# Optimization experiments

Measured on AMD Instinct MI355X. Metric: run time of the kernel, lower is better.

Reference implementation:

```python
import jax, jax.numpy as jnp
import numpy as np
import jax.scipy.linalg as jsl

EPS = 1e-3
GROUP_SIZE = 16

def setup_inputs() -> dict:
    key = jax.random.key(0)
    x = jax.random.normal(key, (32, 512, 56, 56), dtype=jnp.float32)
    return {"x": x}

def reference(x):
    B, C, H, W = x.shape
    gs = GROUP_SIZE
    G = C // gs
    # batch mean per channel: mean over (B, H, W)
    m = jnp.mean(x, axis=(0, 2, 3), keepdims=True)  # [1, C, 1, 1]
    xn = x - m
    # [C, B, H, W] -> [G, gs, N] with N = B*H*W
    T = jnp.transpose(xn, (1, 0, 2, 3)).reshape(G, gs, -1)
    N = T.shape[-1]
    f_cov = jnp.einsum('gin,gjn->gij', T, T) / N  # [G, gs, gs]
    eye = jnp.eye(gs, dtype=x.dtype)
    f_cov_shrinked = (1.0 - EPS) * f_cov + EPS * eye
    L = jnp.linalg.cholesky(f_cov_shrinked)  # lower triangular, L L^T = cov
    # inverse of L via triangular solve against identity (batched)
    Linv = jsl.solve_triangular(L, jnp.broadcast_to(eye, (G, gs, gs)), lower=True)
    # grouped 1x1 conv == per-group matmul: out_g = Linv_g @ xn_g
    dec = jnp.einsum('gij,gjn->gin', Linv, T)  # [G, gs, N]
    out = jnp.transpose(dec.reshape(C, B, H, W), (1, 0, 2, 3))
    return out
```

## Files before the change

kernel.cpp:

```cpp
#include <hip/hip_runtime.h>
#include <hip/hip_bf16.h>
#include <math.h>

#define Bb 32
#define Cc 512
#define HW 3136
#define HW4 784
#define G  32
#define GS 16
#define Nn (Bb*HW)
#define EPSF 1e-3f
#define TRI 136
#define STATS (TRI+GS)

typedef float floatx4 __attribute__((ext_vector_type(4)));

#define TIDX(i,j) ((i)*GS - (i)*((i)+1)/2 + (j))

__global__ __launch_bounds__(256) void stats_kernel(const float* __restrict__ x,
                                                    float* __restrict__ part) {
    const int blk = blockIdx.x;
    const int b = blk / G;
    const int g = blk % G;
    const float* base = x + ((size_t)b * Cc + (size_t)g * GS) * HW;

    float s[GS];
    float c[TRI];
#pragma unroll
    for (int i = 0; i < GS; i++) s[i] = 0.f;
#pragma unroll
    for (int i = 0; i < TRI; i++) c[i] = 0.f;

    for (int p = threadIdx.x; p < HW; p += 256) {
        float v[GS];
#pragma unroll
        for (int j = 0; j < GS; j++) v[j] = base[(size_t)j * HW + p];
#pragma unroll
        for (int j = 0; j < GS; j++) s[j] += v[j];
#pragma unroll
        for (int i = 0; i < GS; i++) {
#pragma unroll
            for (int j = i; j < GS; j++) {
                c[TIDX(i, j)] += v[i] * v[j];
            }
        }
    }

#pragma unroll
    for (int m = 1; m < 64; m <<= 1) {
#pragma unroll
        for (int i = 0; i < GS; i++) s[i] += __shfl_xor(s[i], m, 64);
#pragma unroll
        for (int i = 0; i < TRI; i++) c[i] += __shfl_xor(c[i], m, 64);
    }

    __shared__ float red[4][STATS];
    const int wave = threadIdx.x >> 6;
    const int lane = threadIdx.x & 63;
    if (lane == 0) {
#pragma unroll
        for (int i = 0; i < GS; i++) red[wave][i] = s[i];
#pragma unroll
        for (int i = 0; i < TRI; i++) red[wave][GS + i] = c[i];
    }
    __syncthreads();
    if (threadIdx.x < STATS) {
        float t = red[0][threadIdx.x] + red[1][threadIdx.x] +
                  red[2][threadIdx.x] + red[3][threadIdx.x];
        part[((size_t)g * Bb + b) * STATS + threadIdx.x] = t;
    }
}

__global__ __launch_bounds__(64) void solve_kernel(const float* __restrict__ part,
                                                   float* __restrict__ wl) {
    const int g = blockIdx.x;
    const int t = threadIdx.x;

    __shared__ float st[STATS];
    __shared__ float cov[GS][GS];
    __shared__ float L[GS][GS];
    __shared__ float Li[GS][GS];
    __shared__ float m[GS];

    for (int k = t; k < STATS; k += 64) {
        float acc = 0.f;
#pragma unroll
        for (int b = 0; b < Bb; b++)
            acc += part[((size_t)g * Bb + b) * STATS + k];
        st[k] = acc;
    }
    __syncthreads();

    if (t < GS) m[t] = st[t] * (1.0f / (float)Nn);
    __syncthreads();

    for (int e = t; e < GS * GS; e += 64) {
        int i = e >> 4, j = e & 15;
        int ii = i < j ? i : j;
        int jj = i < j ? j : i;
        float cv = st[GS + TIDX(ii, jj)] * (1.0f / (float)Nn) - m[i] * m[j];
        cv *= (1.0f - EPSF);
        if (i == j) cv += EPSF;
        cov[i][j] = cv;
    }
    __syncthreads();

    if (t == 0) {
        for (int k = 0; k < GS; k++) {
            float d = cov[k][k];
            for (int r = 0; r < k; r++) d -= L[k][r] * L[k][r];
            d = sqrtf(d);
            L[k][k] = d;
            float inv = 1.0f / d;
            for (int i = k + 1; i < GS; i++) {
                float v = cov[i][k];
                for (int r = 0; r < k; r++) v -= L[i][r] * L[k][r];
                L[i][k] = v * inv;
            }
        }
    }
    __syncthreads();

    if (t < GS) {
        const int j = t;
        for (int i = 0; i < GS; i++) Li[i][j] = 0.f;
        for (int i = j; i < GS; i++) {
            float v = (i == j) ? 1.f : 0.f;
            for (int k = j; k < i; k++) v -= L[i][k] * Li[k][j];
            Li[i][j] = v / L[i][i];
        }
    }
    __syncthreads();

    float* wg = wl + (size_t)g * STATS;
    for (int e = t; e < GS * GS; e += 64) {
        int i = e >> 4, j = e & 15;
        if (j <= i) wg[i * (i + 1) / 2 + j] = Li[i][j];
    }
    if (t < GS) {
        float bias = 0.f;
        for (int j = 0; j <= t; j++) bias += Li[t][j] * m[j];
        wg[TRI + t] = bias;
    }
}

__global__ __launch_bounds__(256) void apply_kernel(const float* __restrict__ x,
                                                    const float* __restrict__ wl,
                                                    float* __restrict__ out) {
    const int blk = blockIdx.x;
    const int b = blk / G;
    const int g = blk % G;

    const float* __restrict__ wg = wl + (size_t)g * STATS;
    float Lt[TRI];
    float bias[GS];
#pragma unroll
    for (int i = 0; i < TRI; i++) Lt[i] = wg[i];
#pragma unroll
    for (int i = 0; i < GS; i++) bias[i] = wg[TRI + i];

    const size_t base_off = ((size_t)b * Cc + (size_t)g * GS) * HW;
    const floatx4* __restrict__ xb4 = reinterpret_cast<const floatx4*>(x + base_off);
    floatx4* __restrict__ ob4 = reinterpret_cast<floatx4*>(out + base_off);

    for (int p = threadIdx.x; p < HW4; p += 256) {
        floatx4 v[GS];
#pragma unroll
        for (int j = 0; j < GS; j++) v[j] = xb4[(size_t)j * HW4 + p];
#pragma unroll
        for (int i = 0; i < GS; i++) {
            floatx4 o = (floatx4)(-bias[i]);
#pragma unroll
            for (int j = 0; j <= i; j++) {
                o += Lt[i * (i + 1) / 2 + j] * v[j];
            }
            __builtin_nontemporal_store(o, &ob4[(size_t)i * HW4 + p]);
        }
    }
}

extern "C" void kernel_launch(void* const* d_in, const int* in_sizes, int n_in,
                              void* d_out, int out_size, void* d_ws, size_t ws_size,
                              hipStream_t stream) {
    const float* x = (const float*)d_in[0];
    float* out = (float*)d_out;

    float* part = (float*)d_ws;
    float* wl = part + (size_t)G * Bb * STATS;

    stats_kernel<<<Bb * G, 256, 0, stream>>>(x, part);
    solve_kernel<<<G, 64, 0, stream>>>(part, wl);
    apply_kernel<<<Bb * G, 256, 0, stream>>>(x, wl, out);
}
```

Baseline: 431.5 us.

## Vectorize stats loads, parallelize Cholesky via shuffles, stage weights in LDS

The stats kernel now loads float4 vectors and accumulates the covariance with explicit FMAs over four pixels per thread. This cuts the number of load instructions, and each thread now covers 784 float4 positions instead of 3136 scalars. The solve kernel replaces the single-thread Cholesky with a 16-lane, register-based factorization that uses wave shuffles, and moves the triangular inverse into unrolled registers. The apply kernel reads its weights from shared memory instead of holding 152 values in registers. Both big kernels get a launch_bounds hint of 2 blocks per CU, which risks register spills in the stats kernel with its 152 accumulators.

```diff
diff --git a/kernel.cpp b/kernel.cpp
--- a/kernel.cpp
+++ b/kernel.cpp
@@ -17,12 +17,13 @@
 
 #define TIDX(i,j) ((i)*GS - (i)*((i)+1)/2 + (j))
 
-__global__ __launch_bounds__(256) void stats_kernel(const float* __restrict__ x,
-                                                    float* __restrict__ part) {
+__global__ __launch_bounds__(256, 2) void stats_kernel(const float* __restrict__ x,
+                                                       float* __restrict__ part) {
     const int blk = blockIdx.x;
     const int b = blk / G;
     const int g = blk % G;
-    const float* base = x + ((size_t)b * Cc + (size_t)g * GS) * HW;
+    const floatx4* __restrict__ xb4 = reinterpret_cast<const floatx4*>(
+        x + ((size_t)b * Cc + (size_t)g * GS) * HW);
 
     float s[GS];
     float c[TRI];
@@ -31,17 +32,22 @@
 #pragma unroll
     for (int i = 0; i < TRI; i++) c[i] = 0.f;
 
-    for (int p = threadIdx.x; p < HW; p += 256) {
-        float v[GS];
-#pragma unroll
-        for (int j = 0; j < GS; j++) v[j] = base[(size_t)j * HW + p];
-#pragma unroll
-        for (int j = 0; j < GS; j++) s[j] += v[j];
+    for (int p = threadIdx.x; p < HW4; p += 256) {
+        floatx4 v[GS];
+#pragma unroll
+        for (int j = 0; j < GS; j++) v[j] = xb4[(size_t)j * HW4 + p];
+#pragma unroll
+        for (int j = 0; j < GS; j++) s[j] += (v[j].x + v[j].y) + (v[j].z + v[j].w);
 #pragma unroll
         for (int i = 0; i < GS; i++) {
 #pragma unroll
             for (int j = i; j < GS; j++) {
-                c[TIDX(i, j)] += v[i] * v[j];
+                float acc = c[TIDX(i, j)];
+                acc = fmaf(v[i].x, v[j].x, acc);
+                acc = fmaf(v[i].y, v[j].y, acc);
+                acc = fmaf(v[i].z, v[j].z, acc);
+                acc = fmaf(v[i].w, v[j].w, acc);
+                c[TIDX(i, j)] = acc;
             }
         }
     }
@@ -77,10 +83,8 @@
     const int t = threadIdx.x;
 
     __shared__ float st[STATS];
-    __shared__ float cov[GS][GS];
-    __shared__ float L[GS][GS];
-    __shared__ float Li[GS][GS];
-    __shared__ float m[GS];
+    __shared__ float Lsh[GS][GS + 1];
+    __shared__ float Ish[GS][GS + 1];
 
     for (int k = t; k < STATS; k += 64) {
         float acc = 0.f;
@@ -91,73 +95,83 @@
     }
     __syncthreads();
 
-    if (t < GS) m[t] = st[t] * (1.0f / (float)Nn);
-    __syncthreads();
-
-    for (int e = t; e < GS * GS; e += 64) {
-        int i = e >> 4, j = e & 15;
-        int ii = i < j ? i : j;
-        int jj = i < j ? j : i;
-        float cv = st[GS + TIDX(ii, jj)] * (1.0f / (float)Nn) - m[i] * m[j];
-        cv *= (1.0f - EPSF);
-        if (i == j) cv += EPSF;
-        cov[i][j] = cv;
-    }
-    __syncthreads();
-
-    if (t == 0) {
+    const float invN = 1.0f / (float)Nn;
+
+    if (t < GS) {
+        float A[GS];
+        const float mi = st[t] * invN;
+#pragma unroll
+        for (int j = 0; j < GS; j++) {
+            const int ii = t < j ? t : j;
+            const int jj = t < j ? j : t;
+            const float mj = st[j] * invN;
+            float cv = st[GS + TIDX(ii, jj)] * invN - mi * mj;
+            cv *= (1.0f - EPSF);
+            if (j == t) cv += EPSF;
+            A[j] = cv;
+        }
+
+#pragma unroll
         for (int k = 0; k < GS; k++) {
-            float d = cov[k][k];
-            for (int r = 0; r < k; r++) d -= L[k][r] * L[k][r];
-            d = sqrtf(d);
-            L[k][k] = d;
-            float inv = 1.0f / d;
-            for (int i = k + 1; i < GS; i++) {
-                float v = cov[i][k];
-                for (int r = 0; r < k; r++) v -= L[i][r] * L[k][r];
-                L[i][k] = v * inv;
+            const float dkk = __shfl(A[k], k, 64);
+            const float d = sqrtf(dkk);
+            const float lik = (t == k) ? d : A[k] / d;
+            A[k] = lik;
+#pragma unroll
+            for (int j = k + 1; j < GS; j++) {
+                const float ljk = __shfl(A[k], j, 64);
+                A[j] -= lik * ljk;
             }
         }
+
+#pragma unroll
+        for (int j = 0; j < GS; j++) Lsh[t][j] = A[j];
     }
     __syncthreads();
 
     if (t < GS) {
         const int j = t;
-        for (int i = 0; i < GS; i++) Li[i][j] = 0.f;
-        for (int i = j; i < GS; i++) {
+        float col[GS];
+#pragma unroll
+        for (int i = 0; i < GS; i++) col[i] = 0.f;
+#pragma unroll
+        for (int i = 0; i < GS; i++) {
             float v = (i == j) ? 1.f : 0.f;
-            for (int k = j; k < i; k++) v -= L[i][k] * Li[k][j];
-            Li[i][j] = v / L[i][i];
-        }
+#pragma unroll
+            for (int k = 0; k < i; k++) v -= Lsh[i][k] * col[k];
+            col[i] = (i >= j) ? v / Lsh[i][i] : 0.f;
+        }
+#pragma unroll
+        for (int i = 0; i < GS; i++) Ish[i][j] = col[i];
     }
     __syncthreads();
 
     float* wg = wl + (size_t)g * STATS;
     for (int e = t; e < GS * GS; e += 64) {
-        int i = e >> 4, j = e & 15;
-        if (j <= i) wg[i * (i + 1) / 2 + j] = Li[i][j];
+        const int i = e >> 4, j = e & 15;
+        if (j <= i) wg[i * (i + 1) / 2 + j] = Ish[i][j];
     }
     if (t < GS) {
         float bias = 0.f;
-        for (int j = 0; j <= t; j++) bias += Li[t][j] * m[j];
+#pragma unroll
+        for (int j = 0; j < GS; j++) bias += Ish[t][j] * (st[j] * invN);
         wg[TRI + t] = bias;
     }
 }
 
-__global__ __launch_bounds__(256) void apply_kernel(const float* __restrict__ x,
-                                                    const float* __restrict__ wl,
-                                                    float* __restrict__ out) {
+__global__ __launch_bounds__(256, 2) void apply_kernel(const float* __restrict__ x,
+                                                       const float* __restrict__ wl,
+                                                       float* __restrict__ out) {
     const int blk = blockIdx.x;
     const int b = blk / G;
     const int g = blk % G;
 
-    const float* __restrict__ wg = wl + (size_t)g * STATS;
-    float Lt[TRI];
-    float bias[GS];
-#pragma unroll
-    for (int i = 0; i < TRI; i++) Lt[i] = wg[i];
-#pragma unroll
-    for (int i = 0; i < GS; i++) bias[i] = wg[TRI + i];
+    __shared__ float Ls[STATS];
+    {
+        const float* __restrict__ wg = wl + (size_t)g * STATS;
+        for (int i = threadIdx.x; i < STATS; i += 256) Ls[i] = wg[i];
+    }
+    __syncthreads();
 
     const size_t base_off = ((size_t)b * Cc + (size_t)g * GS) * HW;
     const floatx4* __restrict__ xb4 = reinterpret_cast<const floatx4*>(x + base_off);
@@ -169,10 +183,10 @@
         for (int j = 0; j < GS; j++) v[j] = xb4[(size_t)j * HW4 + p];
 #pragma unroll
         for (int i = 0; i < GS; i++) {
-            floatx4 o = (floatx4)(-bias[i]);
+            floatx4 o = (floatx4)(-Ls[TRI + i]);
 #pragma unroll
             for (int j = 0; j <= i; j++) {
-                o += Lt[i * (i + 1) / 2 + j] * v[j];
+                o += Ls[i * (i + 1) / 2 + j] * v[j];
             }
             __builtin_nontemporal_store(o, &ob4[(size_t)i * HW4 + p]);
         }
```

Result: slower. 1.331 ms (+208.3%).
